# Kernel optimization log

Measured on AMD Instinct MI355X. Metric: run time of the kernel, lower is better.

## Reference

```python
import jax, jax.numpy as jnp
import numpy as np

B, T, C = 1, 2048, 1024
H, HKV, DH, WIN = 16, 4, 64, 128
EPS = 1e-5


def rotate_half(x):
    x1, x2 = jnp.split(x, 2, axis=-1)
    return jnp.concatenate((-x2, x1), axis=-1)


def setup_inputs() -> dict:
    key = jax.random.key(0)
    ks = jax.random.split(key, 8)
    s = 0.02
    return {
        "x": jax.random.normal(ks[0], (B, T, C), dtype=jnp.float32),
        "Wq": jax.random.normal(ks[1], (C, H * DH), dtype=jnp.float32) * s,
        "Wk": jax.random.normal(ks[2], (C, HKV * DH), dtype=jnp.float32) * s,
        "Wv": jax.random.normal(ks[3], (C, HKV * DH), dtype=jnp.float32) * s,
        "Wc": jax.random.normal(ks[4], (C, C), dtype=jnp.float32) * s,
        "Wg": jax.random.normal(ks[5], (C, H), dtype=jnp.float32) * s,
        "bg": jax.random.normal(ks[6], (H,), dtype=jnp.float32) * s,
        "rms_w": jnp.ones((C,), dtype=jnp.float32),
    }


def reference(x, Wq, Wk, Wv, Wc, Wg, bg, rms_w):
    n_rep = H // HKV
    # projections -> [B, heads, T, DH]
    q = (x @ Wq).reshape(B, T, H, DH).transpose(0, 2, 1, 3)
    k = (x @ Wk).reshape(B, T, HKV, DH).transpose(0, 2, 1, 3)
    v = (x @ Wv).reshape(B, T, HKV, DH).transpose(0, 2, 1, 3)
    # rotary embedding (freqs duplicated across the two halves)
    inv_freq = 1.0 / (10000.0 ** (jnp.arange(0, DH, 2, dtype=jnp.float32) / DH))
    freqs = jnp.arange(T, dtype=jnp.float32)[:, None] * inv_freq[None, :]
    emb = jnp.concatenate((freqs, freqs), axis=-1)  # [T, DH]
    cos, sin = jnp.cos(emb)[None, None], jnp.sin(emb)[None, None]
    q = q * cos + rotate_half(q) * sin
    k = k * cos + rotate_half(k) * sin
    # GQA: repeat kv heads (contiguous repeat matches torch expand+reshape)
    k = jnp.repeat(k, n_rep, axis=1)
    v = jnp.repeat(v, n_rep, axis=1)
    # gated decay
    gate_logits = (x @ Wg + bg).reshape(B, T, H, 1).transpose(0, 2, 1, 3)  # [B,H,T,1]
    log_alpha = jax.nn.log_sigmoid(gate_logits)
    log_in_scale = jax.nn.log_sigmoid(-gate_logits)
    k_scaled = k * jnp.exp(log_in_scale)
    la_cum = jnp.cumsum(log_alpha, axis=2)                  # [B,H,T,1]
    log_decay = la_cum - jnp.swapaxes(la_cum, 2, 3)         # [B,H,T,T]
    causal = jnp.triu(jnp.ones((T, T), dtype=bool), k=1)
    decay = jnp.exp(jnp.where(causal, -jnp.inf, log_decay))
    scores = jnp.einsum('bhtd,bhsd->bhts', q, k_scaled)
    y_global = jnp.einsum('bhts,bhsd->bhtd', scores * decay, v)
    nb = T // WIN
    qb = q.reshape(B, H, nb, WIN, DH)
    kb = k.reshape(B, H, nb, WIN, DH)
    vb = v.reshape(B, H, nb, WIN, DH)
    att = jnp.einsum('bhnqd,bhnkd->bhnqk', qb, kb) / jnp.sqrt(jnp.float32(DH))
    wmask = jnp.triu(jnp.ones((WIN, WIN), dtype=bool), k=1)
    att = jax.nn.softmax(jnp.where(wmask, -jnp.inf, att), axis=-1)
    y_local = jnp.einsum('bhnqk,bhnkd->bhnqd', att, vb).reshape(B, H, T, DH)
    # fuse, RMSNorm, output projection
    y = (y_global + y_local).transpose(0, 2, 1, 3).reshape(B, T, C)
    y = y * jax.lax.rsqrt(jnp.mean(y * y, axis=-1, keepdims=True) + EPS) * rms_w
    return y @ Wc
```

## Files before the change

kernel.cpp:

```cpp
#include <hip/hip_runtime.h>
#include <hip/hip_bf16.h>


typedef __attribute__((ext_vector_type(8))) short bf16x8;
typedef __attribute__((ext_vector_type(4))) float f32x4;

#define MFMA16(a, b, c) __builtin_amdgcn_mfma_f32_16x16x32_bf16(a, b, c, 0, 0, 0)
#define LN10000_OVER_32 0.28782313662425575f

__device__ __forceinline__ short f2b(float f) {
  __hip_bfloat16 h = __float2bfloat16(f);
  return *reinterpret_cast<short*>(&h);
}
__device__ __forceinline__ float b2f(short s) {
  return __uint_as_float(((unsigned)(unsigned short)s) << 16);
}
__device__ __forceinline__ void gload16(const void* g, void* l) {
  __builtin_amdgcn_global_load_lds(
      (const __attribute__((address_space(1))) void*)g,
      (__attribute__((address_space(3))) void*)l, 16, 0, 0);
}

__device__ __forceinline__ void transpose_cvt_body(
    const float* __restrict__ src, short* __restrict__ dst, int R, int C,
    int bx, int by, float* ts , const float* __restrict__ sw) {
  int c0 = bx * 32, r0 = by * 32;
  int tr = threadIdx.x >> 3, tc = (threadIdx.x & 7) * 4;
  float4 v = *(const float4*)&src[(size_t)(r0 + tr) * C + c0 + tc];
  ts[tr * 33 + tc] = v.x;
  ts[tr * 33 + tc + 1] = v.y;
  ts[tr * 33 + tc + 2] = v.z;
  ts[tr * 33 + tc + 3] = v.w;
  __syncthreads();
  alignas(8) short o[4];
#pragma unroll
  for (int i = 0; i < 4; ++i) {
    float m = sw ? sw[r0 + tc + i] : 1.0f;
    o[i] = f2b(ts[(tc + i) * 33 + tr] * m);
  }
  *(uint2*)&dst[(size_t)(c0 + tr) * R + r0 + tc] = *(uint2*)o;
}

__global__ __launch_bounds__(256) void prep_fused(
    const float* __restrict__ x, const float* __restrict__ Wq,
    const float* __restrict__ Wk, const float* __restrict__ Wv,
    const float* __restrict__ Wc, const float* __restrict__ Wg,
    const float* __restrict__ bg, const float* __restrict__ rmsw,
    short* __restrict__ xb, short* __restrict__ wqkvT,
    short* __restrict__ wcT, float* __restrict__ g, float* __restrict__ rs) {
  __shared__ float ts[32 * 33];
  const int j = blockIdx.x;
  const int tid = threadIdx.x;
  if (j < 2048) {
    const int t = j;
    const int h = tid & 15, chunk = tid >> 4;
    const float* xr = x + (size_t)t * 1024 + chunk * 64;
    const float* wg = Wg + (size_t)chunk * 64 * 16 + h;
    float acc = 0.f;
#pragma unroll
    for (int c = 0; c < 64; c += 4) {
      float4 xv = *(const float4*)(xr + c);
      acc = fmaf(xv.x, wg[(c + 0) * 16], acc);
      acc = fmaf(xv.y, wg[(c + 1) * 16], acc);
      acc = fmaf(xv.z, wg[(c + 2) * 16], acc);
      acc = fmaf(xv.w, wg[(c + 3) * 16], acc);
    }
    ts[chunk * 16 + h] = acc;
    __syncthreads();
    if (tid < 16) {
      float s = bg[tid];
#pragma unroll
      for (int i = 0; i < 16; ++i) s += ts[i * 16 + tid];
      g[t * 16 + tid] = s;
    }
  } else if (j < 3072) {
    int i = ((j - 2048) * 256 + tid) * 8;
    float4 a = *(const float4*)(x + i);
    float4 b = *(const float4*)(x + i + 4);
    alignas(16) short o[8] = {f2b(a.x), f2b(a.y), f2b(a.z), f2b(a.w),
                              f2b(b.x), f2b(b.y), f2b(b.z), f2b(b.w)};
    *(float4*)(xb + i) = *(float4*)o;
  } else if (j < 4096) {
    int jj = j - 3072;
    transpose_cvt_body(Wq, wqkvT, 1024, 1024, jj & 31, jj >> 5, ts, nullptr);
  } else if (j < 4352) {
    int jj = j - 4096;
    transpose_cvt_body(Wk, wqkvT + 1024 * 1024, 1024, 256, jj & 7, jj >> 3, ts,
                       nullptr);
  } else if (j < 4608) {
    int jj = j - 4352;
    transpose_cvt_body(Wv, wqkvT + 1280 * 1024, 1024, 256, jj & 7, jj >> 3, ts,
                       nullptr);
  } else if (j < 5632) {
    int jj = j - 4608;
    transpose_cvt_body(Wc, wcT, 1024, 1024, jj & 31, jj >> 5, ts, rmsw);
  } else {
    int i4 = ((j - 5632) * 256 + tid) * 4;
    float4 z = {0.f, 0.f, 0.f, 0.f};
    *(float4*)(rs + i4) = z;
  }
}

__global__ __launch_bounds__(256) void qkv_gemm_fused(
    const short* __restrict__ A, const short* __restrict__ Bt,
    short* __restrict__ qkvb, short* __restrict__ vtb,
    short* __restrict__ ktb, const float* __restrict__ g,
    float* __restrict__ lac, float* __restrict__ insc) {
  __shared__ short As[128 * 64];
  __shared__ short Bs[64 * 64];
  __shared__ float part[256];
  const int id = blockIdx.x;
  const int tid = threadIdx.x;
  if (id >= 384) {
    const int h = id - 384;
    float vals[8];
    float local = 0.f;
#pragma unroll
    for (int i = 0; i < 8; ++i) {
      int t = tid * 8 + i;
      float gv = g[t * 16 + h];
      float la = (gv > 0.f) ? -log1pf(expf(-gv)) : (gv - log1pf(expf(gv)));
      insc[h * 2048 + t] = 1.f / (1.f + expf(gv));
      vals[i] = la;
      local += la;
    }
    part[tid] = local;
    __syncthreads();
    for (int off = 1; off < 256; off <<= 1) {
      float add = (tid >= off) ? part[tid - off] : 0.f;
      __syncthreads();
      part[tid] += add;
      __syncthreads();
    }
    float run = (tid > 0) ? part[tid - 1] : 0.f;
#pragma unroll
    for (int i = 0; i < 8; ++i) {
      run += vals[i];
      lac[h * 2048 + tid * 8 + i] = run;
    }
    return;
  }
  const int lane = tid & 63, wid = tid >> 6;
  const int l15 = lane & 15, lq = lane >> 4;
  const int jlin = id >> 3;
  const int by = (id & 7) + 8 * (jlin / 24);
  const int bx = jlin % 24;
  const int m0 = by * 128, n0 = bx * 64;
  const int K = 1024;
  const int srow = lane >> 3;
  const int sc16 = (lane & 7) ^ srow;
  f32x4 acc[2][4];
#pragma unroll
  for (int mt = 0; mt < 2; ++mt)
#pragma unroll
    for (int nt = 0; nt < 4; ++nt) acc[mt][nt] = {0.f, 0.f, 0.f, 0.f};
  for (int kt = 0; kt < K; kt += 64) {
    __syncthreads();
#pragma unroll
    for (int i = 0; i < 4; ++i) {
      int jj = wid * 4 + i;
      int row = jj * 8 + srow;
      gload16(A + (size_t)(m0 + row) * K + kt + sc16 * 8, &As[jj * 512]);
    }
#pragma unroll
    for (int i = 0; i < 2; ++i) {
      int jj = wid * 2 + i;
      int row = jj * 8 + srow;
      gload16(Bt + (size_t)(n0 + row) * K + kt + sc16 * 8, &Bs[jj * 512]);
    }
    __syncthreads();
    bf16x8 af[2][2], bfr[4][2];
#pragma unroll
    for (int ks = 0; ks < 2; ++ks) {
      int c16 = ks * 4 + lq;
#pragma unroll
      for (int mt = 0; mt < 2; ++mt) {
        int ar = wid * 32 + mt * 16 + l15;
        af[mt][ks] = *(const bf16x8*)&As[(ar * 8 + (c16 ^ (ar & 7))) * 8];
      }
#pragma unroll
      for (int nt = 0; nt < 4; ++nt) {
        int br = nt * 16 + l15;
        bfr[nt][ks] = *(const bf16x8*)&Bs[(br * 8 + (c16 ^ (br & 7))) * 8];
      }
    }
#pragma unroll
    for (int ks = 0; ks < 2; ++ks)
#pragma unroll
      for (int mt = 0; mt < 2; ++mt)
#pragma unroll
        for (int nt = 0; nt < 4; ++nt)
          acc[mt][nt] = MFMA16(af[mt][ks], bfr[nt][ks], acc[mt][nt]);
  }
  if (bx >= 20) {
#pragma unroll
    for (int mt = 0; mt < 2; ++mt) {
      int row0 = m0 + wid * 32 + mt * 16 + lq * 4;
#pragma unroll
      for (int nt = 0; nt < 4; ++nt) {
        int vcol = (n0 - 1280) + nt * 16 + l15;
        alignas(8) short o4[4];
#pragma unroll
        for (int r = 0; r < 4; ++r) o4[r] = f2b(acc[mt][nt][r]);
        *(uint2*)&vtb[(size_t)vcol * 2048 + row0] = *(uint2*)o4;
      }
    }
    return;
  }
  const bool isk = (bx >= 16);
#pragma unroll
  for (int mt = 0; mt < 2; ++mt) {
    int row0 = m0 + wid * 32 + mt * 16 + lq * 4;
#pragma unroll
    for (int nt = 0; nt < 2; ++nt) {
      int d = nt * 16 + l15;
      float ivf = __expf(-LN10000_OVER_32 * (float)d);
      alignas(8) short oa[4], ob[4];
#pragma unroll
      for (int r = 0; r < 4; ++r) {
        int row_g = row0 + r;
        float th = (float)row_g * ivf;
        float cs = cosf(th), sn = sinf(th);
        float a = acc[mt][nt][r], b = acc[mt][nt + 2][r];
        oa[r] = f2b(a * cs - b * sn);
        ob[r] = f2b(b * cs + a * sn);
        qkvb[(size_t)row_g * 1536 + n0 + d] = oa[r];
        qkvb[(size_t)row_g * 1536 + n0 + d + 32] = ob[r];
      }
      if (isk) {
        int dk = n0 - 1024 + d;
        *(uint2*)&ktb[(size_t)dk * 2048 + row0] = *(uint2*)oa;
        *(uint2*)&ktb[(size_t)(dk + 32) * 2048 + row0] = *(uint2*)ob;
      }
    }
  }
}

__global__ __launch_bounds__(256) void chunk_state(
    const short* __restrict__ vtb, const short* __restrict__ ktb,
    const float* __restrict__ lac, const float* __restrict__ insc,
    float* __restrict__ Bmat) {
  __shared__ short Ks[64 * 64], Vts[64 * 64];
  __shared__ float lacs[64], inss[64], gvals[64];
  const int tid = threadIdx.x, lane = tid & 63, wid = tid >> 6;
  const int l15 = lane & 15, lq = lane >> 4;
  const int h = blockIdx.y, kh = h >> 2, c = blockIdx.x;
  const int srow = lane >> 3;
  const int sc16 = (lane & 7) ^ srow;
#pragma unroll
  for (int i = 0; i < 2; ++i) {
    int jj = wid * 2 + i;
    int row = jj * 8 + srow;
    gload16(ktb + (size_t)(kh * 64 + row) * 2048 + c * 64 + sc16 * 8,
            &Ks[jj * 512]);
    gload16(vtb + (size_t)(kh * 64 + row) * 2048 + c * 64 + sc16 * 8,
            &Vts[jj * 512]);
  }
  if (tid < 64) {
    lacs[tid] = lac[h * 2048 + c * 64 + tid];
    inss[tid] = insc[h * 2048 + c * 64 + tid];
  }
  __syncthreads();
  if (tid < 64)
    gvals[tid] = __expf(fminf(lacs[63] - lacs[tid], 0.f)) * inss[tid];
  __syncthreads();
  const int er = wid * 16 + l15;
  bf16x8 av[2];
#pragma unroll
  for (int ks = 0; ks < 2; ++ks) {
    int c16 = ks * 4 + lq;
    bf16x8 raw = *(const bf16x8*)&Vts[(er * 8 + (c16 ^ (er & 7))) * 8];
    float4 g0 = *(const float4*)&gvals[c16 * 8];
    float4 g1 = *(const float4*)&gvals[c16 * 8 + 4];
    float gv[8] = {g0.x, g0.y, g0.z, g0.w, g1.x, g1.y, g1.z, g1.w};
    bf16x8 sc;
#pragma unroll
    for (int jx = 0; jx < 8; ++jx) sc[jx] = f2b(b2f(raw[jx]) * gv[jx]);
    av[ks] = sc;
  }
  f32x4 acc[4];
#pragma unroll
  for (int nt = 0; nt < 4; ++nt) acc[nt] = {0.f, 0.f, 0.f, 0.f};
#pragma unroll
  for (int ks = 0; ks < 2; ++ks) {
    int c16 = ks * 4 + lq;
#pragma unroll
    for (int nt = 0; nt < 4; ++nt) {
      int dr = nt * 16 + l15;
      bf16x8 bk = *(const bf16x8*)&Ks[(dr * 8 + (c16 ^ (dr & 7))) * 8];
      acc[nt] = MFMA16(av[ks], bk, acc[nt]);
    }
  }
  float* Bout = Bmat + (size_t)(h * 32 + c) * 4096;
#pragma unroll
  for (int nt = 0; nt < 4; ++nt)
#pragma unroll
    for (int r = 0; r < 4; ++r) {
      int e = wid * 16 + lq * 4 + r;
      Bout[e * 64 + nt * 16 + l15] = acc[nt][r];
    }
}

__global__ __launch_bounds__(256) void scan_kernel(
    const float* __restrict__ Bmat, const float* __restrict__ lac,
    short* __restrict__ St) {
  const int h = blockIdx.x, sl = blockIdx.y, tid = threadIdx.x;
  __shared__ float lacE[32];
  if (tid < 32) lacE[tid] = lac[h * 2048 + tid * 64 + 63];
  __syncthreads();
  const int base = sl * 512 + tid * 2;
  float S0 = 0.f, S1 = 0.f;
  *(unsigned*)&St[(size_t)(h * 32) * 4096 + base] = 0u;
  float2 p = *(const float2*)(Bmat + (size_t)(h * 32) * 4096 + base);
  for (int c = 1; c < 32; ++c) {
    float2 n = p;
    if (c < 31) n = *(const float2*)(Bmat + (size_t)(h * 32 + c) * 4096 + base);
    float a = (c >= 2) ? __expf(fminf(lacE[c - 1] - lacE[c - 2], 0.f)) : 0.f;
    S0 = fmaf(a, S0, p.x);
    S1 = fmaf(a, S1, p.y);
    unsigned pack = (unsigned)(unsigned short)f2b(S0) |
                    ((unsigned)(unsigned short)f2b(S1) << 16);
    *(unsigned*)&St[(size_t)(h * 32 + c) * 4096 + base] = pack;
    p = n;
  }
}

__global__ __launch_bounds__(256) void fused_attn(
    const short* __restrict__ qkv, const short* __restrict__ vtb,
    const short* __restrict__ St, const float* __restrict__ lac,
    const float* __restrict__ insc, short* __restrict__ ys,
    float* __restrict__ rs) {
  const int c = blockIdx.x, h = blockIdx.y;
  const int kh = h >> 2;
  const bool odd = (c & 1) != 0;
  __shared__ short Qs[64 * 64], Kd[64 * 64], Vd[64 * 64], Sts[64 * 64],
      Kp[64 * 64], Vp[64 * 64], Pd[64 * 64], Pp[64 * 64];
  __shared__ float lacq[64], inss[64];
  __shared__ float laprev_sh;
  const int tid = threadIdx.x, lane = tid & 63, wid = tid >> 6;
  const int l15 = lane & 15, lq = lane >> 4;
  const int srow = lane >> 3;
  const int sc16 = (lane & 7) ^ srow;
#pragma unroll
  for (int i = 0; i < 2; ++i) {
    int jj = wid * 2 + i;
    int row = jj * 8 + srow;
    gload16(qkv + (size_t)(c * 64 + row) * 1536 + h * 64 + sc16 * 8,
            &Qs[jj * 512]);
    gload16(qkv + (size_t)(c * 64 + row) * 1536 + 1024 + kh * 64 + sc16 * 8,
            &Kd[jj * 512]);
    gload16(vtb + (size_t)(kh * 64 + row) * 2048 + c * 64 + sc16 * 8,
            &Vd[jj * 512]);
    gload16(St + (size_t)(h * 32 + c) * 4096 + row * 64 + sc16 * 8,
            &Sts[jj * 512]);
  }
  if (odd) {
#pragma unroll
    for (int i = 0; i < 2; ++i) {
      int jj = wid * 2 + i;
      int row = jj * 8 + srow;
      gload16(qkv + (size_t)((c - 1) * 64 + row) * 1536 + 1024 + kh * 64 +
                  sc16 * 8,
              &Kp[jj * 512]);
      gload16(vtb + (size_t)(kh * 64 + row) * 2048 + (c - 1) * 64 + sc16 * 8,
              &Vp[jj * 512]);
    }
  }
  if (tid < 64) {
    lacq[tid] = lac[h * 2048 + c * 64 + tid];
    inss[tid] = insc[h * 2048 + c * 64 + tid];
  }
  if (tid == 0) laprev_sh = (c > 0) ? lac[h * 2048 + c * 64 - 1] : 1e30f;
  __syncthreads();
  const int qr = wid * 16 + l15;
  bf16x8 aq[2];
#pragma unroll
  for (int ks = 0; ks < 2; ++ks) {
    int c16 = ks * 4 + lq;
    aq[ks] = *(const bf16x8*)&Qs[(qr * 8 + (c16 ^ (qr & 7))) * 8];
  }
  f32x4 sv[4];
#pragma unroll
  for (int nt = 0; nt < 4; ++nt) {
    int kr = nt * 16 + l15;
    bf16x8 bk0 = *(const bf16x8*)&Kd[(kr * 8 + ((0 + lq) ^ (kr & 7))) * 8];
    bf16x8 bk1 = *(const bf16x8*)&Kd[(kr * 8 + ((4 + lq) ^ (kr & 7))) * 8];
    f32x4 z = {0.f, 0.f, 0.f, 0.f};
    z = MFMA16(aq[0], bk0, z);
    z = MFMA16(aq[1], bk1, z);
    sv[nt] = z;
  }
  f32x4 sp[4];
  if (odd) {
#pragma unroll
    for (int nt = 0; nt < 4; ++nt) {
      int kr = nt * 16 + l15;
      bf16x8 bk0 = *(const bf16x8*)&Kp[(kr * 8 + ((0 + lq) ^ (kr & 7))) * 8];
      bf16x8 bk1 = *(const bf16x8*)&Kp[(kr * 8 + ((4 + lq) ^ (kr & 7))) * 8];
      f32x4 z = {0.f, 0.f, 0.f, 0.f};
      z = MFMA16(aq[0], bk0, z);
      z = MFMA16(aq[1], bk1, z);
      sp[nt] = z;
    }
  } else {
#pragma unroll
    for (int nt = 0; nt < 4; ++nt) sp[nt] = {0.f, 0.f, 0.f, 0.f};
  }
  f32x4 oi[4];
#pragma unroll
  for (int nt = 0; nt < 4; ++nt) {
    int er = nt * 16 + l15;
    bf16x8 bs0 = *(const bf16x8*)&Sts[(er * 8 + ((0 + lq) ^ (er & 7))) * 8];
    bf16x8 bs1 = *(const bf16x8*)&Sts[(er * 8 + ((4 + lq) ^ (er & 7))) * 8];
    f32x4 z = {0.f, 0.f, 0.f, 0.f};
    z = MFMA16(aq[0], bs0, z);
    z = MFMA16(aq[1], bs1, z);
    oi[nt] = z;
  }
  float mrow[4], ssum[4];
  float vd[4][4], vp[4][4];
#pragma unroll
  for (int r = 0; r < 4; ++r) mrow[r] = -1e30f;
#pragma unroll
  for (int nt = 0; nt < 4; ++nt) {
    int col = nt * 16 + l15;
#pragma unroll
    for (int r = 0; r < 4; ++r) {
      int row = wid * 16 + lq * 4 + r;
      float xv = (col <= row) ? sv[nt][r] * 0.125f : -1e30f;
      vd[nt][r] = xv;
      mrow[r] = fmaxf(mrow[r], xv);
      if (odd) {
        float xp = sp[nt][r] * 0.125f;
        vp[nt][r] = xp;
        mrow[r] = fmaxf(mrow[r], xp);
      }
    }
  }
#pragma unroll
  for (int r = 0; r < 4; ++r) {
    for (int off = 1; off < 16; off <<= 1)
      mrow[r] = fmaxf(mrow[r], __shfl_xor(mrow[r], off, 64));
    ssum[r] = 0.f;
  }
#pragma unroll
  for (int nt = 0; nt < 4; ++nt) {
#pragma unroll
    for (int r = 0; r < 4; ++r) {
      float e = __expf(vd[nt][r] - mrow[r]);
      vd[nt][r] = e;
      ssum[r] += e;
      if (odd) {
        float ep = __expf(vp[nt][r] - mrow[r]);
        vp[nt][r] = ep;
        ssum[r] += ep;
      }
    }
  }
#pragma unroll
  for (int r = 0; r < 4; ++r) {
    for (int off = 1; off < 16; off <<= 1) ssum[r] += __shfl_xor(ssum[r], off, 64);
    ssum[r] = 1.f / ssum[r];
  }
#pragma unroll
  for (int nt = 0; nt < 4; ++nt) {
    int col = nt * 16 + l15;
    float ls = lacq[col], is = inss[col];
#pragma unroll
    for (int r = 0; r < 4; ++r) {
      int row = wid * 16 + lq * 4 + r;
      float w = __expf(fminf(lacq[row] - ls, 0.f)) * is;
      if (col > row) w = 0.f;
      float pc = sv[nt][r] * w + vd[nt][r] * ssum[r];
      Pd[(row * 8 + ((col >> 3) ^ (row & 7))) * 8 + (col & 7)] = f2b(pc);
      if (odd)
        Pp[(row * 8 + ((col >> 3) ^ (row & 7))) * 8 + (col & 7)] =
            f2b(vp[nt][r] * ssum[r]);
    }
  }
  __syncthreads();
  bf16x8 ap[2];
#pragma unroll
  for (int ks = 0; ks < 2; ++ks) {
    int c16 = ks * 4 + lq;
    ap[ks] = *(const bf16x8*)&Pd[(qr * 8 + (c16 ^ (qr & 7))) * 8];
  }
  f32x4 o[4];
#pragma unroll
  for (int nt = 0; nt < 4; ++nt) {
    int vr = nt * 16 + l15;
    bf16x8 bv0 = *(const bf16x8*)&Vd[(vr * 8 + ((0 + lq) ^ (vr & 7))) * 8];
    bf16x8 bv1 = *(const bf16x8*)&Vd[(vr * 8 + ((4 + lq) ^ (vr & 7))) * 8];
    f32x4 z = {0.f, 0.f, 0.f, 0.f};
    z = MFMA16(ap[0], bv0, z);
    z = MFMA16(ap[1], bv1, z);
    o[nt] = z;
  }
  if (odd) {
    bf16x8 app[2];
#pragma unroll
    for (int ks = 0; ks < 2; ++ks) {
      int c16 = ks * 4 + lq;
      app[ks] = *(const bf16x8*)&Pp[(qr * 8 + (c16 ^ (qr & 7))) * 8];
    }
#pragma unroll
    for (int nt = 0; nt < 4; ++nt) {
      int vr = nt * 16 + l15;
      bf16x8 bv0 = *(const bf16x8*)&Vp[(vr * 8 + ((0 + lq) ^ (vr & 7))) * 8];
      bf16x8 bv1 = *(const bf16x8*)&Vp[(vr * 8 + ((4 + lq) ^ (vr & 7))) * 8];
      o[nt] = MFMA16(app[0], bv0, o[nt]);
      o[nt] = MFMA16(app[1], bv1, o[nt]);
    }
  }
  const float laprev = laprev_sh;
#pragma unroll
  for (int r = 0; r < 4; ++r) {
    int row = wid * 16 + lq * 4 + r;
    float rfac = __expf(fminf(lacq[row] - laprev, 0.f));
    int row_g = c * 64 + row;
    float ssq = 0.f;
#pragma unroll
    for (int nt = 0; nt < 4; ++nt) {
      int colg = h * 64 + nt * 16 + l15;
      size_t idx = (size_t)row_g * 1024 + colg;
      float v = o[nt][r] + rfac * oi[nt][r];
      ys[idx] = f2b(v);
      ssq = fmaf(v, v, ssq);
    }
    for (int off = 1; off < 16; off <<= 1) ssq += __shfl_xor(ssq, off, 64);
    if (l15 == 0) atomicAdd(&rs[row_g], ssq);
  }
}

__global__ __launch_bounds__(256) void out_gemm(
    const short* __restrict__ A, const short* __restrict__ Bt,
    const float* __restrict__ rs, float* __restrict__ C) {
  __shared__ short As[64 * 64];
  __shared__ short Bs[64 * 64];
  const int tid = threadIdx.x, lane = tid & 63, wid = tid >> 6;
  const int l15 = lane & 15, lq = lane >> 4;
  const int wm = wid >> 1, wn = wid & 1;
  const int id = blockIdx.x;
  const int jlin = id >> 3;
  const int by = (id & 7) + 8 * (jlin / 16);
  const int bx = jlin % 16;
  const int m0 = by * 64, n0 = bx * 64;
  const int K = 1024;
  const int srow = lane >> 3;
  const int sc16 = (lane & 7) ^ srow;
  f32x4 acc[2][2];
#pragma unroll
  for (int mt = 0; mt < 2; ++mt)
#pragma unroll
    for (int nt = 0; nt < 2; ++nt) acc[mt][nt] = {0.f, 0.f, 0.f, 0.f};
  for (int kt = 0; kt < K; kt += 64) {
    __syncthreads();
#pragma unroll
    for (int i = 0; i < 2; ++i) {
      int jj = wid * 2 + i;
      int row = jj * 8 + srow;
      gload16(A + (size_t)(m0 + row) * K + kt + sc16 * 8, &As[jj * 512]);
      gload16(Bt + (size_t)(n0 + row) * K + kt + sc16 * 8, &Bs[jj * 512]);
    }
    __syncthreads();
    bf16x8 af[2][2], bfr[2][2];
#pragma unroll
    for (int ks = 0; ks < 2; ++ks) {
      int c16 = ks * 4 + lq;
#pragma unroll
      for (int mt = 0; mt < 2; ++mt) {
        int ar = wm * 32 + mt * 16 + l15;
        af[mt][ks] = *(const bf16x8*)&As[(ar * 8 + (c16 ^ (ar & 7))) * 8];
      }
#pragma unroll
      for (int nt = 0; nt < 2; ++nt) {
        int br = wn * 32 + nt * 16 + l15;
        bfr[nt][ks] = *(const bf16x8*)&Bs[(br * 8 + (c16 ^ (br & 7))) * 8];
      }
    }
#pragma unroll
    for (int ks = 0; ks < 2; ++ks)
#pragma unroll
      for (int mt = 0; mt < 2; ++mt)
#pragma unroll
        for (int nt = 0; nt < 2; ++nt)
          acc[mt][nt] = MFMA16(af[mt][ks], bfr[nt][ks], acc[mt][nt]);
  }
#pragma unroll
  for (int mt = 0; mt < 2; ++mt) {
    int row0 = m0 + wm * 32 + mt * 16 + lq * 4;
#pragma unroll
    for (int r = 0; r < 4; ++r) {
      int row_g = row0 + r;
      float sc = rsqrtf(rs[row_g] * (1.0f / 1024.0f) + 1e-5f);
#pragma unroll
      for (int nt = 0; nt < 2; ++nt)
        C[(size_t)row_g * 1024 + n0 + wn * 32 + nt * 16 + l15] =
            acc[mt][nt][r] * sc;
    }
  }
}

extern "C" void kernel_launch(void* const* d_in, const int* in_sizes, int n_in,
                              void* d_out, int out_size, void* d_ws,
                              size_t ws_size, hipStream_t stream) {
  const float* x = (const float*)d_in[0];
  const float* Wq = (const float*)d_in[1];
  const float* Wk = (const float*)d_in[2];
  const float* Wv = (const float*)d_in[3];
  const float* Wc = (const float*)d_in[4];
  const float* Wg = (const float*)d_in[5];
  const float* bg = (const float*)d_in[6];
  const float* rmsw = (const float*)d_in[7];
  float* out = (float*)d_out;

  short* wqkvT = (short*)d_ws;
  short* wcT = wqkvT + 1536 * 1024;
  short* qkvb = wcT + 1024 * 1024;
  short* vtb = qkvb + 2048 * 1536;
  short* ktb = vtb + 256 * 2048;
  float* gw = (float*)(ktb + 256 * 2048);
  float* lacw = gw + 2048 * 16;
  float* inscw = lacw + 16 * 2048;
  float* Bmat = inscw + 16 * 2048;
  short* Stb = (short*)(Bmat + 16 * 32 * 4096);
  short* xb = Stb + 16 * 32 * 4096;
  short* ys = xb;
  short* ylc = xb + 2048 * 1024;
  float* rsq = (float*)(ylc + 2048 * 1024);

  prep_fused<<<5634, 256, 0, stream>>>(x, Wq, Wk, Wv, Wc, Wg, bg, rmsw, xb,
                                       wqkvT, wcT, gw, rsq);
  qkv_gemm_fused<<<400, 256, 0, stream>>>(xb, wqkvT, qkvb, vtb, ktb, gw, lacw,
                                          inscw);
  chunk_state<<<dim3(32, 16), 256, 0, stream>>>(vtb, ktb, lacw, inscw, Bmat);
  scan_kernel<<<dim3(16, 8), 256, 0, stream>>>(Bmat, lacw, Stb);
  fused_attn<<<dim3(32, 16), 256, 0, stream>>>(qkvb, vtb, Stb, lacw, inscw,
                                               ys, rsq);
  out_gemm<<<512, 256, 0, stream>>>(ys, wcT, rsq, out);
}
```

Baseline: 133.7 us.

## Enlarge GEMM tiles for QKV and output projections, store chunk states in bf16

New measurement: 176.3 us. +31.9%, slower.

```diff
diff --git a/kernel.cpp b/kernel.cpp
--- a/kernel.cpp
+++ b/kernel.cpp
@@ -106,13 +106,13 @@
     short* __restrict__ qkvb, short* __restrict__ vtb,
     short* __restrict__ ktb, const float* __restrict__ g,
     float* __restrict__ lac, float* __restrict__ insc) {
-  __shared__ short As[128 * 64];
+  __shared__ short As[256 * 64];
   __shared__ short Bs[64 * 64];
   __shared__ float part[256];
   const int id = blockIdx.x;
   const int tid = threadIdx.x;
-  if (id >= 384) {
-    const int h = id - 384;
+  if (id >= 192) {
+    const int h = id - 192;
     float vals[8];
     float local = 0.f;
 #pragma unroll
@@ -142,23 +142,22 @@
   }
   const int lane = tid & 63, wid = tid >> 6;
   const int l15 = lane & 15, lq = lane >> 4;
-  const int jlin = id >> 3;
-  const int by = (id & 7) + 8 * (jlin / 24);
-  const int bx = jlin % 24;
-  const int m0 = by * 128, n0 = bx * 64;
+  const int by = id & 7;
+  const int bx = id >> 3;
+  const int m0 = by * 256, n0 = bx * 64;
   const int K = 1024;
   const int srow = lane >> 3;
   const int sc16 = (lane & 7) ^ srow;
-  f32x4 acc[2][4];
-#pragma unroll
-  for (int mt = 0; mt < 2; ++mt)
+  f32x4 acc[4][4];
+#pragma unroll
+  for (int mt = 0; mt < 4; ++mt)
 #pragma unroll
     for (int nt = 0; nt < 4; ++nt) acc[mt][nt] = {0.f, 0.f, 0.f, 0.f};
   for (int kt = 0; kt < K; kt += 64) {
     __syncthreads();
 #pragma unroll
-    for (int i = 0; i < 4; ++i) {
-      int jj = wid * 4 + i;
+    for (int i = 0; i < 8; ++i) {
+      int jj = wid * 8 + i;
       int row = jj * 8 + srow;
       gload16(A + (size_t)(m0 + row) * K + kt + sc16 * 8, &As[jj * 512]);
     }
@@ -169,33 +168,31 @@
       gload16(Bt + (size_t)(n0 + row) * K + kt + sc16 * 8, &Bs[jj * 512]);
     }
     __syncthreads();
-    bf16x8 af[2][2], bfr[4][2];
 #pragma unroll
     for (int ks = 0; ks < 2; ++ks) {
       int c16 = ks * 4 + lq;
-#pragma unroll
-      for (int mt = 0; mt < 2; ++mt) {
-        int ar = wid * 32 + mt * 16 + l15;
-        af[mt][ks] = *(const bf16x8*)&As[(ar * 8 + (c16 ^ (ar & 7))) * 8];
+      bf16x8 af[4], bfr[4];
+#pragma unroll
+      for (int mt = 0; mt < 4; ++mt) {
+        int ar = wid * 64 + mt * 16 + l15;
+        af[mt] = *(const bf16x8*)&As[(ar * 8 + (c16 ^ (ar & 7))) * 8];
       }
 #pragma unroll
       for (int nt = 0; nt < 4; ++nt) {
         int br = nt * 16 + l15;
-        bfr[nt][ks] = *(const bf16x8*)&Bs[(br * 8 + (c16 ^ (br & 7))) * 8];
-      }
-    }
-#pragma unroll
-    for (int ks = 0; ks < 2; ++ks)
-#pragma unroll
-      for (int mt = 0; mt < 2; ++mt)
+        bfr[nt] = *(const bf16x8*)&Bs[(br * 8 + (c16 ^ (br & 7))) * 8];
+      }
+#pragma unroll
+      for (int mt = 0; mt < 4; ++mt)
 #pragma unroll
         for (int nt = 0; nt < 4; ++nt)
-          acc[mt][nt] = MFMA16(af[mt][ks], bfr[nt][ks], acc[mt][nt]);
+          acc[mt][nt] = MFMA16(af[mt], bfr[nt], acc[mt][nt]);
+    }
   }
   if (bx >= 20) {
 #pragma unroll
-    for (int mt = 0; mt < 2; ++mt) {
-      int row0 = m0 + wid * 32 + mt * 16 + lq * 4;
+    for (int mt = 0; mt < 4; ++mt) {
+      int row0 = m0 + wid * 64 + mt * 16 + lq * 4;
 #pragma unroll
       for (int nt = 0; nt < 4; ++nt) {
         int vcol = (n0 - 1280) + nt * 16 + l15;
@@ -209,8 +206,8 @@
   }
   const bool isk = (bx >= 16);
 #pragma unroll
-  for (int mt = 0; mt < 2; ++mt) {
-    int row0 = m0 + wid * 32 + mt * 16 + lq * 4;
+  for (int mt = 0; mt < 4; ++mt) {
+    int row0 = m0 + wid * 64 + mt * 16 + lq * 4;
 #pragma unroll
     for (int nt = 0; nt < 2; ++nt) {
       int d = nt * 16 + l15;
@@ -239,7 +236,7 @@
 __global__ __launch_bounds__(256) void chunk_state(
     const short* __restrict__ vtb, const short* __restrict__ ktb,
     const float* __restrict__ lac, const float* __restrict__ insc,
-    float* __restrict__ Bmat) {
+    short* __restrict__ Bmat) {
   __shared__ short Ks[64 * 64], Vts[64 * 64];
   __shared__ float lacs[64], inss[64], gvals[64];
   const int tid = threadIdx.x, lane = tid & 63, wid = tid >> 6;
@@ -291,18 +288,18 @@
       acc[nt] = MFMA16(av[ks], bk, acc[nt]);
     }
   }
-  float* Bout = Bmat + (size_t)(h * 32 + c) * 4096;
+  short* Bout = Bmat + (size_t)(h * 32 + c) * 4096;
 #pragma unroll
   for (int nt = 0; nt < 4; ++nt)
 #pragma unroll
     for (int r = 0; r < 4; ++r) {
       int e = wid * 16 + lq * 4 + r;
-      Bout[e * 64 + nt * 16 + l15] = acc[nt][r];
+      Bout[e * 64 + nt * 16 + l15] = f2b(acc[nt][r]);
     }
 }
 
 __global__ __launch_bounds__(256) void scan_kernel(
-    const float* __restrict__ Bmat, const float* __restrict__ lac,
+    const short* __restrict__ Bmat, const float* __restrict__ lac,
     short* __restrict__ St) {
   const int h = blockIdx.x, sl = blockIdx.y, tid = threadIdx.x;
   __shared__ float lacE[32];
@@ -311,13 +308,14 @@
   const int base = sl * 512 + tid * 2;
   float S0 = 0.f, S1 = 0.f;
   *(unsigned*)&St[(size_t)(h * 32) * 4096 + base] = 0u;
-  float2 p = *(const float2*)(Bmat + (size_t)(h * 32) * 4096 + base);
+  unsigned p = *(const unsigned*)&Bmat[(size_t)(h * 32) * 4096 + base];
   for (int c = 1; c < 32; ++c) {
-    float2 n = p;
-    if (c < 31) n = *(const float2*)(Bmat + (size_t)(h * 32 + c) * 4096 + base);
+    unsigned n = p;
+    if (c < 31)
+      n = *(const unsigned*)&Bmat[(size_t)(h * 32 + c) * 4096 + base];
     float a = (c >= 2) ? __expf(fminf(lacE[c - 1] - lacE[c - 2], 0.f)) : 0.f;
-    S0 = fmaf(a, S0, p.x);
-    S1 = fmaf(a, S1, p.y);
+    S0 = fmaf(a, S0, b2f((short)(p & 0xffffu)));
+    S1 = fmaf(a, S1, b2f((short)(p >> 16)));
     unsigned pack = (unsigned)(unsigned short)f2b(S0) |
                     ((unsigned)(unsigned short)f2b(S1) << 16);
     *(unsigned*)&St[(size_t)(h * 32 + c) * 4096 + base] = pack;
@@ -535,68 +533,68 @@
 __global__ __launch_bounds__(256) void out_gemm(
     const short* __restrict__ A, const short* __restrict__ Bt,
     const float* __restrict__ rs, float* __restrict__ C) {
-  __shared__ short As[64 * 64];
+  __shared__ short As[128 * 64];
   __shared__ short Bs[64 * 64];
   const int tid = threadIdx.x, lane = tid & 63, wid = tid >> 6;
   const int l15 = lane & 15, lq = lane >> 4;
-  const int wm = wid >> 1, wn = wid & 1;
   const int id = blockIdx.x;
-  const int jlin = id >> 3;
-  const int by = (id & 7) + 8 * (jlin / 16);
-  const int bx = jlin % 16;
-  const int m0 = by * 64, n0 = bx * 64;
+  const int by = (id & 7) + 8 * (id >> 7);
+  const int bx = (id >> 3) & 15;
+  const int m0 = by * 128, n0 = bx * 64;
   const int K = 1024;
   const int srow = lane >> 3;
   const int sc16 = (lane & 7) ^ srow;
-  f32x4 acc[2][2];
+  f32x4 acc[2][4];
 #pragma unroll
   for (int mt = 0; mt < 2; ++mt)
 #pragma unroll
-    for (int nt = 0; nt < 2; ++nt) acc[mt][nt] = {0.f, 0.f, 0.f, 0.f};
+    for (int nt = 0; nt < 4; ++nt) acc[mt][nt] = {0.f, 0.f, 0.f, 0.f};
   for (int kt = 0; kt < K; kt += 64) {
     __syncthreads();
+#pragma unroll
+    for (int i = 0; i < 4; ++i) {
+      int jj = wid * 4 + i;
+      int row = jj * 8 + srow;
+      gload16(A + (size_t)(m0 + row) * K + kt + sc16 * 8, &As[jj * 512]);
+    }
 #pragma unroll
     for (int i = 0; i < 2; ++i) {
       int jj = wid * 2 + i;
       int row = jj * 8 + srow;
-      gload16(A + (size_t)(m0 + row) * K + kt + sc16 * 8, &As[jj * 512]);
       gload16(Bt + (size_t)(n0 + row) * K + kt + sc16 * 8, &Bs[jj * 512]);
     }
     __syncthreads();
-    bf16x8 af[2][2], bfr[2][2];
 #pragma unroll
     for (int ks = 0; ks < 2; ++ks) {
       int c16 = ks * 4 + lq;
+      bf16x8 af[2], bfr[4];
 #pragma unroll
       for (int mt = 0; mt < 2; ++mt) {
-        int ar = wm * 32 + mt * 16 + l15;
-        af[mt][ks] = *(const bf16x8*)&As[(ar * 8 + (c16 ^ (ar & 7))) * 8];
-      }
-#pragma unroll
-      for (int nt = 0; nt < 2; ++nt) {
-        int br = wn * 32 + nt * 16 + l15;
-        bfr[nt][ks] = *(const bf16x8*)&Bs[(br * 8 + (c16 ^ (br & 7))) * 8];
-      }
-    }
-#pragma unroll
-    for (int ks = 0; ks < 2; ++ks)
+        int ar = wid * 32 + mt * 16 + l15;
+        af[mt] = *(const bf16x8*)&As[(ar * 8 + (c16 ^ (ar & 7))) * 8];
+      }
+#pragma unroll
+      for (int nt = 0; nt < 4; ++nt) {
+        int br = nt * 16 + l15;
+        bfr[nt] = *(const bf16x8*)&Bs[(br * 8 + (c16 ^ (br & 7))) * 8];
+      }
 #pragma unroll
       for (int mt = 0; mt < 2; ++mt)
 #pragma unroll
-        for (int nt = 0; nt < 2; ++nt)
-          acc[mt][nt] = MFMA16(af[mt][ks], bfr[nt][ks], acc[mt][nt]);
+        for (int nt = 0; nt < 4; ++nt)
+          acc[mt][nt] = MFMA16(af[mt], bfr[nt], acc[mt][nt]);
+    }
   }
 #pragma unroll
   for (int mt = 0; mt < 2; ++mt) {
-    int row0 = m0 + wm * 32 + mt * 16 + lq * 4;
+    int row0 = m0 + wid * 32 + mt * 16 + lq * 4;
 #pragma unroll
     for (int r = 0; r < 4; ++r) {
       int row_g = row0 + r;
       float sc = rsqrtf(rs[row_g] * (1.0f / 1024.0f) + 1e-5f);
 #pragma unroll
-      for (int nt = 0; nt < 2; ++nt)
-        C[(size_t)row_g * 1024 + n0 + wn * 32 + nt * 16 + l15] =
-            acc[mt][nt][r] * sc;
+      for (int nt = 0; nt < 4; ++nt)
+        C[(size_t)row_g * 1024 + n0 + nt * 16 + l15] = acc[mt][nt][r] * sc;
     }
   }
 }
@@ -622,20 +620,19 @@
   float* gw = (float*)(ktb + 256 * 2048);
   float* lacw = gw + 2048 * 16;
   float* inscw = lacw + 16 * 2048;
-  float* Bmat = inscw + 16 * 2048;
-  short* Stb = (short*)(Bmat + 16 * 32 * 4096);
+  short* Bmat = (short*)(inscw + 16 * 2048);
+  short* Stb = Bmat + 16 * 32 * 4096;
   short* xb = Stb + 16 * 32 * 4096;
   short* ys = xb;
-  short* ylc = xb + 2048 * 1024;
-  float* rsq = (float*)(ylc + 2048 * 1024);
+  float* rsq = (float*)(xb + 2048 * 1024);
 
   prep_fused<<<5634, 256, 0, stream>>>(x, Wq, Wk, Wv, Wc, Wg, bg, rmsw, xb,
                                        wqkvT, wcT, gw, rsq);
-  qkv_gemm_fused<<<400, 256, 0, stream>>>(xb, wqkvT, qkvb, vtb, ktb, gw, lacw,
+  qkv_gemm_fused<<<208, 256, 0, stream>>>(xb, wqkvT, qkvb, vtb, ktb, gw, lacw,
                                           inscw);
   chunk_state<<<dim3(32, 16), 256, 0, stream>>>(vtb, ktb, lacw, inscw, Bmat);
   scan_kernel<<<dim3(16, 8), 256, 0, stream>>>(Bmat, lacw, Stb);
   fused_attn<<<dim3(32, 16), 256, 0, stream>>>(qkvb, vtb, Stb, lacw, inscw,
                                                ys, rsq);
-  out_gemm<<<512, 256, 0, stream>>>(ys, wcT, rsq, out);
-}
+  out_gemm<<<256, 256, 0, stream>>>(ys, wcT, rsq, out);
+}
```
